# Kernel tuning notes

Hardware: AMD Instinct MI355X
Metric: run time of the kernel (lower is better)

## Reference

```python
import jax, jax.numpy as jnp
import numpy as np

N_NODES = 163842
N_EDGES = 983040
NUM_FEATURES = 22
LAYER_SIZES = [22, 32, 64, 64]
K = 3  # kernel_size
D = 2  # pseudo-coordinate dim
EPS = 1e-15


def _glorot(key, shape):
    fan = shape[0] + shape[-1]
    s = jnp.sqrt(6.0 / fan)
    return jax.random.uniform(key, shape, jnp.float32, -s, s)


def setup_inputs() -> dict:
    key = jax.random.key(0)
    ks = iter(jax.random.split(key, 64))
    inp = {
        'x': jax.random.normal(next(ks), (N_NODES, NUM_FEATURES), jnp.float32),
        'edge_index': jax.random.randint(next(ks), (2, N_EDGES), 0, N_NODES, jnp.int64),
        'edge_attr': jax.random.uniform(next(ks), (N_EDGES, D), jnp.float32),
    }
    for i, (cin, cout) in enumerate(zip(LAYER_SIZES[:-1], LAYER_SIZES[1:])):
        inp[f'g{i}'] = _glorot(next(ks), (cin, K * cout))
        inp[f'mu{i}'] = _glorot(next(ks), (K, D))
        inp[f'sigma{i}'] = jax.random.uniform(next(ks), (K, D), jnp.float32, 0.5, 1.5)
        inp[f'root{i}'] = _glorot(next(ks), (cin, cout))
        inp[f'b{i}'] = jnp.zeros((cout,), jnp.float32)
    inp['fc_w'] = _glorot(next(ks), (LAYER_SIZES[-1], 2))
    inp['fc_b'] = jnp.zeros((2,), jnp.float32)
    return inp


def gmm_conv(x, src, dst, pseudo, g, mu, sigma, root, bias):
    # PyG GMMConv, separate_gaussians=False, aggr='mean', root_weight=True
    n = x.shape[0]
    cout = root.shape[1]
    xw = (x @ g).reshape(n, K, cout)                       # [N, K, Cout]
    diff = pseudo[:, None, :] - mu[None, :, :]             # [E, K, D]
    gauss = jnp.exp(-0.5 * jnp.sum(diff * diff / (EPS + sigma[None] ** 2), axis=-1))  # [E, K]
    msg = jnp.einsum('ek,eko->eo', gauss, xw[src])         # [E, Cout]
    agg = jax.ops.segment_sum(msg, dst, num_segments=n)
    deg = jax.ops.segment_sum(jnp.ones((src.shape[0],), x.dtype), dst, num_segments=n)
    agg = agg / jnp.clip(deg, 1.0)[:, None]                # mean aggregation
    return agg + x @ root + bias


def reference(x, edge_index, edge_attr, g0, mu0, sigma0, root0, b0,
              g1, mu1, sigma1, root1, b1, g2, mu2, sigma2, root2, b2,
              fc_w, fc_b):
    src, dst = edge_index[0], edge_index[1]
    params = [(g0, mu0, sigma0, root0, b0),
              (g1, mu1, sigma1, root1, b1),
              (g2, mu2, sigma2, root2, b2)]
    h = x
    for (g, mu, sigma, root, b) in params:
        h = jax.nn.relu(gmm_conv(h, src, dst, edge_attr, g, mu, sigma, root, b))
    logits = h @ fc_w + fc_b                               # [N, 2]
    return jax.nn.log_softmax(logits, axis=1)
```

## Files before the change

### kernel.cpp

```cpp
#include <hip/hip_runtime.h>

#define NN 163842
#define NE 983040
#define NBIN 641
#define BINCAP 2048

using short8   = __attribute__((ext_vector_type(8))) short;
using ushort8v = __attribute__((ext_vector_type(8))) unsigned short;
using f32x4    = __attribute__((ext_vector_type(4))) float;
using v2f      = __attribute__((ext_vector_type(2))) float;

static __device__ __forceinline__ unsigned short bf16rne(float x) {
    unsigned u = __float_as_uint(x);
    u += 0x7FFFu + ((u >> 16) & 1u);
    return (unsigned short)(u >> 16);
}

static __device__ __forceinline__ v2f bfpair(unsigned u) {
    v2f r;
    r[0] = __uint_as_float(u << 16);
    r[1] = __uint_as_float(u & 0xffff0000u);
    return r;
}

__global__ __launch_bounds__(256) void bin_pass(const int* __restrict__ dst,
                                                const int* __restrict__ src,
                                                const float* __restrict__ ea,
                                                int* __restrict__ bincnt,
                                                int4* __restrict__ binbuf) {
    __shared__ int hist[NBIN], base[NBIN], pos[NBIN];
    const int t = threadIdx.x;
    for (int i = t; i < NBIN; i += 256) { hist[i] = 0; pos[i] = 0; }
    __syncthreads();
    const int e0 = blockIdx.x * 7680;
#pragma unroll 2
    for (int it = 0; it < 30; ++it) {
        int b = dst[e0 + it * 256 + t] >> 8;
        atomicAdd(&hist[b], 1);
    }
    __syncthreads();
    for (int i = t; i < NBIN; i += 256)
        if (hist[i] > 0) base[i] = atomicAdd(&bincnt[i], hist[i]);
    __syncthreads();
    for (int it = 0; it < 30; ++it) {
        int e = e0 + it * 256 + t;
        int d = dst[e];
        int b = d >> 8;
        int j = atomicAdd(&pos[b], 1);
        int slot = base[b] + j;
        float2 exy = *(const float2*)(ea + 2 * (size_t)e);
        int4 r;
        r.x = d; r.y = src[e];
        r.z = __float_as_int(exy.x); r.w = __float_as_int(exy.y);
        if (slot < BINCAP) binbuf[(size_t)b * BINCAP + slot] = r;
    }
}

__global__ void scan_bins(const int* __restrict__ bincnt, int* __restrict__ binoff) {
    __shared__ int tmp[1024];
    int t = threadIdx.x;
    int v = (t < NBIN) ? min(bincnt[t], BINCAP) : 0;
    tmp[t] = v;
    __syncthreads();
    for (int o = 1; o < 1024; o <<= 1) {
        int x = (t >= o) ? tmp[t - o] : 0;
        __syncthreads();
        tmp[t] += x;
        __syncthreads();
    }
    if (t < NBIN) binoff[t] = tmp[t] - v;
}

template <int CIN, int CINP, int COUTR>
static __device__ __forceinline__ void wcb_emit(int t, const float* __restrict__ g,
                                                const float* __restrict__ root,
                                                unsigned short* __restrict__ Wcb) {
    constexpr int KTl = 4 * CINP;
    int nIdx = t / KTl, k = t - nIdx * KTl;
    int seg = k / CINP, c = k - seg * CINP;
    float v = 0.0f;
    if (c < CIN)
        v = (seg < 3) ? g[c * (3 * COUTR) + seg * COUTR + nIdx] : root[c * COUTR + nIdx];
    Wcb[t] = bf16rne(v);
}

static __device__ __forceinline__ float3 gauss3c(float ex, float ey,
                                                 const float* muv, const float* ccv) {
    float3 r;
    float dx, dy;
    dx = ex - muv[0]; dy = ey - muv[1];
    r.x = __expf(fmaf(ccv[0] * dx, dx, ccv[1] * dy * dy));
    dx = ex - muv[2]; dy = ey - muv[3];
    r.y = __expf(fmaf(ccv[2] * dx, dx, ccv[3] * dy * dy));
    dx = ex - muv[4]; dy = ey - muv[5];
    r.z = __expf(fmaf(ccv[4] * dx, dx, ccv[5] * dy * dy));
    return r;
}

__global__ __launch_bounds__(256) void build_pass(const int4* __restrict__ binbuf,
                                                  const int* __restrict__ bincnt,
                                                  const int* __restrict__ binoff,
                                                  int* __restrict__ cnt,
                                                  int* __restrict__ cursor,
                                                  const float* __restrict__ mu0, const float* __restrict__ sg0,
                                                  const float* __restrict__ mu1, const float* __restrict__ sg1,
                                                  const float* __restrict__ mu2, const float* __restrict__ sg2,
                                                  float4* __restrict__ ged0,
                                                  float4* __restrict__ ged1,
                                                  float4* __restrict__ ged2,
                                                  const float* __restrict__ x,
                                                  unsigned short* __restrict__ xp,
                                                  const float* __restrict__ g0, const float* __restrict__ rt0,
                                                  const float* __restrict__ g1, const float* __restrict__ rt1,
                                                  const float* __restrict__ g2, const float* __restrict__ rt2,
                                                  unsigned short* __restrict__ W0,
                                                  unsigned short* __restrict__ W1,
                                                  unsigned short* __restrict__ W2,
                                                  int PBLK, int n) {
    __shared__ int h2[256], pre[256], pos2[256];
    const int t = threadIdx.x;
    int bid = blockIdx.x;
    if (bid < NBIN) {
        float muv0[6], ccv0[6], muv1[6], ccv1[6], muv2[6], ccv2[6];
#pragma unroll
        for (int j = 0; j < 6; ++j) {
            muv0[j] = mu0[j]; muv1[j] = mu1[j]; muv2[j] = mu2[j];
            float s0 = sg0[j], s1 = sg1[j], s2 = sg2[j];
            ccv0[j] = -0.5f / (1e-15f + s0 * s0);
            ccv1[j] = -0.5f / (1e-15f + s1 * s1);
            ccv2[j] = -0.5f / (1e-15f + s2 * s2);
        }
        const int total = min(bincnt[bid], BINCAP);
        const int boff  = binoff[bid];
        const int4* bb  = binbuf + (size_t)bid * BINCAP;
        h2[t] = 0; pos2[t] = 0;
        __syncthreads();
        for (int i = t; i < total; i += 256) atomicAdd(&h2[bb[i].x & 255], 1);
        __syncthreads();
        pre[t] = h2[t];
        __syncthreads();
        for (int o = 1; o < 256; o <<= 1) {
            int v = (t >= o) ? pre[t - o] : 0;
            __syncthreads();
            pre[t] += v;
            __syncthreads();
        }
        pre[t] -= h2[t];
        int node = (bid << 8) + t;
        if (node < n) { cnt[node] = h2[t]; cursor[node] = boff + pre[t]; }
        __syncthreads();
        for (int i = t; i < total; i += 256) {
            int4 r = bb[i];
            int l = r.x & 255;
            int j = atomicAdd(&pos2[l], 1);
            int p = boff + pre[l] + j;
            float exf = __int_as_float(r.z), eyf = __int_as_float(r.w);
            float sb  = __int_as_float(r.y);
            float3 G0 = gauss3c(exf, eyf, muv0, ccv0);
            float3 G1 = gauss3c(exf, eyf, muv1, ccv1);
            float3 G2 = gauss3c(exf, eyf, muv2, ccv2);
            ged0[p] = make_float4(sb, G0.x, G0.y, G0.z);
            ged1[p] = make_float4(sb, G1.x, G1.y, G1.z);
            ged2[p] = make_float4(sb, G2.x, G2.y, G2.z);
        }
        return;
    }
    bid -= NBIN;
    if (bid < PBLK) {
        int r = bid * 256 + threadIdx.x;
        if (r >= n) return;
        float v[22];
        const float2* x2 = (const float2*)(x + (size_t)r * 22);
#pragma unroll
        for (int j = 0; j < 11; ++j) *(float2*)(v + 2 * j) = x2[j];
        unsigned short* op = xp + (size_t)r * 32;
#pragma unroll
        for (int g8 = 0; g8 < 4; ++g8) {
            ushort8v o;
#pragma unroll
            for (int j = 0; j < 8; ++j) {
                int c = g8 * 8 + j;
                o[j] = (c < 22) ? bf16rne(v[c]) : (unsigned short)0;
            }
            *(ushort8v*)(op + g8 * 8) = o;
        }
        return;
    }
    bid -= PBLK;
    int tt = bid * 256 + threadIdx.x;
    constexpr int T0 = 32 * 128, T1 = 64 * 128, T2 = 64 * 256;
    if (tt < T0)                wcb_emit<22, 32, 32>(tt, g0, rt0, W0);
    else if (tt < T0 + T1)      wcb_emit<32, 32, 64>(tt - T0, g1, rt1, W1);
    else if (tt < T0 + T1 + T2) wcb_emit<64, 64, 64>(tt - T0 - T1, g2, rt2, W2);
}

template <int CINP, int COUTR, int NT, bool FC>
__global__ __launch_bounds__(NT) void fused_mfma(const unsigned short* __restrict__ h, int hs,
                                                 const float4* __restrict__ ged,
                                                 const int* __restrict__ cursor,
                                                 const int* __restrict__ degi,
                                                 const unsigned short* __restrict__ Wcb,
                                                 const float* __restrict__ bias,
                                                 unsigned short* __restrict__ out,
                                                 const float* __restrict__ fcw,
                                                 const float* __restrict__ fcb,
                                                 float* __restrict__ fout, int n) {
    constexpr int KT    = 4 * CINP;
    constexpr int ST4   = KT / 8 + 1;
    constexpr int ROWU  = ST4 * 8;
    constexpr int NSTEP = KT / 32;
    constexpr int NCT   = COUTR / 16;
    constexpr int LPN   = CINP / 8;
    constexpr int NPP   = NT / LPN;
    static_assert(NPP == 64, "single pass over the 64-node tile");
    __shared__ float4 sa[64 * ST4];
    unsigned short* st = (unsigned short*)sa;
    const int row0 = blockIdx.x * 64;

    {
        const int sub = threadIdx.x / LPN;
        const int li  = threadIdx.x % LPN;
        int node = row0 + sub; if (node > n - 1) node = n - 1;
        int p   = cursor[node];
        int dg  = degi[node];
        int end = p + dg;
        v2f a[3][4];
#pragma unroll
        for (int k = 0; k < 3; ++k)
#pragma unroll
            for (int q = 0; q < 4; ++q) a[k][q] = (v2f){0.0f, 0.0f};
        for (; p < end; p += 4) {
            float4 ed[4];
            uint4  hu[4];
#pragma unroll
            for (int u = 0; u < 4; ++u) {
                int q = p + u;
                ed[u] = ged[(q < end) ? q : (end - 1)];
            }
#pragma unroll
            for (int u = 0; u < 4; ++u)
                hu[u] = *(const uint4*)(h + (long)__float_as_int(ed[u].x) * hs + li * 8);
#pragma unroll
            for (int u = 0; u < 4; ++u)
                if (p + u >= end) { ed[u].y = 0.0f; ed[u].z = 0.0f; ed[u].w = 0.0f; }
#pragma unroll
            for (int u = 0; u < 4; ++u) {
                v2f hv[4] = {bfpair(hu[u].x), bfpair(hu[u].y), bfpair(hu[u].z), bfpair(hu[u].w)};
#pragma unroll
                for (int q = 0; q < 4; ++q) {
                    a[0][q] += hv[q] * ed[u].y;
                    a[1][q] += hv[q] * ed[u].z;
                    a[2][q] += hv[q] * ed[u].w;
                }
            }
        }
        float inv = 1.0f / (float)max(dg, 1);
#pragma unroll
        for (int k = 0; k < 3; ++k)
#pragma unroll
            for (int q = 0; q < 4; ++q) a[k][q] *= inv;
        uint4 hv4 = *(const uint4*)(h + (long)node * hs + li * 8);
        int base = sub * ROWU;
        int c8b  = li * 8;
#pragma unroll
        for (int k = 0; k < 3; ++k) {
            ushort8v v;
#pragma unroll
            for (int q = 0; q < 4; ++q) {
                v[2 * q]     = bf16rne(a[k][q][0]);
                v[2 * q + 1] = bf16rne(a[k][q][1]);
            }
            *(ushort8v*)(st + base + k * CINP + c8b) = v;
        }
        *(uint4*)(st + base + 3 * CINP + c8b) = hv4;
    }
    __syncthreads();

    constexpr int NW    = NT / 64;
    constexpr int TILES = 4 * NCT;
    constexpr int TPW   = TILES / NW;
    constexpr int RST   = NW / NCT;
    static_assert(NW % NCT == 0 && TILES % NW == 0, "tile remap");
    const int lane = threadIdx.x & 63;
    const int wv   = threadIdx.x >> 6;
    const int quad = lane >> 4;
    const int c16  = lane & 15;
    const int ct   = wv % NCT;
    const int rg0  = wv / NCT;
    f32x4 acc[TPW];
#pragma unroll
    for (int i = 0; i < TPW; ++i) acc[i] = (f32x4){0.0f, 0.0f, 0.0f, 0.0f};
    const unsigned short* bcol = Wcb + (ct * 16 + c16) * KT;
#pragma unroll
    for (int s = 0; s < NSTEP; ++s) {
        short8 bf = *(const short8*)(bcol + s * 32 + quad * 8);
#pragma unroll
        for (int i = 0; i < TPW; ++i) {
            const unsigned short* arow = st + (16 * (rg0 + i * RST) + c16) * ROWU;
            short8 af = *(const short8*)(arow + s * 32 + quad * 8);
            acc[i] = __builtin_amdgcn_mfma_f32_16x16x32_bf16(af, bf, acc[i], 0, 0, 0);
        }
    }
    if constexpr (!FC) {
#pragma unroll
        for (int i = 0; i < TPW; ++i) {
            int rg  = rg0 + i * RST;
            int col = ct * 16 + c16;
            float b = bias[col];
#pragma unroll
            for (int r = 0; r < 4; ++r) {
                int grow = row0 + rg * 16 + quad * 4 + r;
                if (grow < n)
                    out[(long)grow * COUTR + col] = bf16rne(fmaxf(acc[i][r] + b, 0.0f));
            }
        }
    } else {
        static_assert(COUTR == 64, "FC fusion assumes 64-wide rows");
        constexpr int FS = 72;
        __syncthreads();
        {
            int col = ct * 16 + c16;
            float b = bias[col];
#pragma unroll
            for (int i = 0; i < TPW; ++i) {
                int rg = rg0 + i * RST;
#pragma unroll
                for (int r = 0; r < 4; ++r) {
                    int lr2 = rg * 16 + quad * 4 + r;
                    st[lr2 * FS + col] = bf16rne(fmaxf(acc[i][r] + b, 0.0f));
                }
            }
        }
        __syncthreads();
        int t = threadIdx.x;
        if (t < 64) {
            int node = row0 + t;
            if (node < n) {
                const ushort8v* hr = (const ushort8v*)(st + t * FS);
                float l0 = fcb[0];
                float l1 = fcb[1];
#pragma unroll
                for (int j8 = 0; j8 < 8; ++j8) {
                    ushort8v hv = hr[j8];
#pragma unroll
                    for (int j = 0; j < 8; ++j) {
                        float hvf = __uint_as_float(((unsigned)hv[j]) << 16);
                        l0 = fmaf(hvf, fcw[2 * (8 * j8 + j)], l0);
                        l1 = fmaf(hvf, fcw[2 * (8 * j8 + j) + 1], l1);
                    }
                }
                float mx  = fmaxf(l0, l1);
                float lse = mx + logf(__expf(l0 - mx) + __expf(l1 - mx));
                fout[2 * (long)node]     = l0 - lse;
                fout[2 * (long)node + 1] = l1 - lse;
            }
        }
    }
}

extern "C" void kernel_launch(void* const* d_in, const int* in_sizes, int n_in,
                              void* d_out, int out_size, void* d_ws, size_t ws_size,
                              hipStream_t stream) {
    const float* x   = (const float*)d_in[0];
    const int*   ei  = (const int*)d_in[1];
    const float* ea  = (const float*)d_in[2];
    const float* g_[3]  = {(const float*)d_in[3],  (const float*)d_in[8],  (const float*)d_in[13]};
    const float* mu_[3] = {(const float*)d_in[4],  (const float*)d_in[9],  (const float*)d_in[14]};
    const float* sg_[3] = {(const float*)d_in[5],  (const float*)d_in[10], (const float*)d_in[15]};
    const float* rt_[3] = {(const float*)d_in[6],  (const float*)d_in[11], (const float*)d_in[16]};
    const float* bs_[3] = {(const float*)d_in[7],  (const float*)d_in[12], (const float*)d_in[17]};
    const float* fcw = (const float*)d_in[18];
    const float* fcb = (const float*)d_in[19];
    float* out = (float*)d_out;
    (void)in_sizes; (void)n_in; (void)out_size; (void)ws_size;

    char* w = (char*)d_ws;
    size_t off = 0;
    auto carve = [&](size_t bytes) -> void* {
        void* p = (void*)(w + off);
        off += (bytes + 255) & ~(size_t)255;
        return p;
    };
    int*    cnt    = (int*)carve((size_t)NN * 4);
    int*    cursor = (int*)carve((size_t)NN * 4);
    int*    bincnt = (int*)carve((size_t)NBIN * 4);
    int*    binoff = (int*)carve((size_t)NBIN * 4);
    float4* ged0   = (float4*)carve((size_t)NE * 16);
    float4* ged1   = (float4*)carve((size_t)NE * 16);
    float4* ged2   = (float4*)carve((size_t)NE * 16);
    unsigned short* W0 = (unsigned short*)carve((size_t)32 * 128 * 2);
    unsigned short* W1 = (unsigned short*)carve((size_t)64 * 128 * 2);
    unsigned short* W2 = (unsigned short*)carve((size_t)64 * 256 * 2);
    unsigned short* xp = (unsigned short*)carve((size_t)NN * 32 * 2);
    char* uni = (char*)carve((size_t)NN * 64 * 2 + (size_t)NN * 32 * 2);
    int4*           binbuf = (int4*)uni;
    unsigned short* hA     = (unsigned short*)uni;
    unsigned short* hB     = (unsigned short*)(uni + (size_t)NN * 32 * 2);

    const int* src = ei;
    const int* dst = ei + NE;
    const int PB = (NN + 255) / 256;
    const int WB = 112;
    const int GB = (NN + 63) / 64;

    hipMemsetAsync(bincnt, 0, (size_t)NBIN * 4, stream);
    bin_pass<<<128, 256, 0, stream>>>(dst, src, ea, bincnt, binbuf);
    scan_bins<<<1, 1024, 0, stream>>>(bincnt, binoff);
    build_pass<<<NBIN + PB + WB, 256, 0, stream>>>(binbuf, bincnt, binoff, cnt, cursor,
                                                   mu_[0], sg_[0], mu_[1], sg_[1], mu_[2], sg_[2],
                                                   ged0, ged1, ged2, x, xp,
                                                   g_[0], rt_[0], g_[1], rt_[1], g_[2], rt_[2],
                                                   W0, W1, W2, PB, NN);

    fused_mfma<32, 32, 256, false><<<GB, 256, 0, stream>>>(xp, 32, ged0, cursor, cnt,
                                                           W0, bs_[0], hA, nullptr, nullptr,
                                                           nullptr, NN);
    fused_mfma<32, 64, 256, false><<<GB, 256, 0, stream>>>(hA, 32, ged1, cursor, cnt,
                                                           W1, bs_[1], hB, nullptr, nullptr,
                                                           nullptr, NN);
    fused_mfma<64, 64, 512, true><<<GB, 512, 0, stream>>>(hB, 64, ged2, cursor, cnt,
                                                          W2, bs_[2], nullptr, fcw, fcb,
                                                          out, NN);
}
```

Measured before the change: 283.0 us.

## Fold bin offset scan into build pass and double bin_pass grid

Removes the separate single-block scan_bins launch. Each build_pass bin block now computes its own offset by reducing the preceding bin counts in shared memory. bin_pass launches twice as many blocks with half the edges each, and the gather loop predicates out-of-range edge and feature loads instead of clamping. This saves one launch and serialization point, at the cost of redundant prefix reads in every bin block.

```diff
diff --git a/kernel.cpp b/kernel.cpp
--- a/kernel.cpp
+++ b/kernel.cpp
@@ -32,9 +32,9 @@
     const int t = threadIdx.x;
     for (int i = t; i < NBIN; i += 256) { hist[i] = 0; pos[i] = 0; }
     __syncthreads();
-    const int e0 = blockIdx.x * 7680;
-#pragma unroll 2
-    for (int it = 0; it < 30; ++it) {
+    const int e0 = blockIdx.x * 3840;
+#pragma unroll 3
+    for (int it = 0; it < 15; ++it) {
         int b = dst[e0 + it * 256 + t] >> 8;
         atomicAdd(&hist[b], 1);
     }
@@ -42,7 +42,7 @@
     for (int i = t; i < NBIN; i += 256)
         if (hist[i] > 0) base[i] = atomicAdd(&bincnt[i], hist[i]);
     __syncthreads();
-    for (int it = 0; it < 30; ++it) {
+    for (int it = 0; it < 15; ++it) {
         int e = e0 + it * 256 + t;
         int d = dst[e];
         int b = d >> 8;
@@ -54,21 +54,6 @@
         r.z = __float_as_int(exy.x); r.w = __float_as_int(exy.y);
         if (slot < BINCAP) binbuf[(size_t)b * BINCAP + slot] = r;
     }
-}
-
-__global__ void scan_bins(const int* __restrict__ bincnt, int* __restrict__ binoff) {
-    __shared__ int tmp[1024];
-    int t = threadIdx.x;
-    int v = (t < NBIN) ? min(bincnt[t], BINCAP) : 0;
-    tmp[t] = v;
-    __syncthreads();
-    for (int o = 1; o < 1024; o <<= 1) {
-        int x = (t >= o) ? tmp[t - o] : 0;
-        __syncthreads();
-        tmp[t] += x;
-        __syncthreads();
-    }
-    if (t < NBIN) binoff[t] = tmp[t] - v;
 }
 
 template <int CIN, int CINP, int COUTR>
@@ -99,7 +84,6 @@
 
 __global__ __launch_bounds__(256) void build_pass(const int4* __restrict__ binbuf,
                                                   const int* __restrict__ bincnt,
-                                                  const int* __restrict__ binoff,
                                                   int* __restrict__ cnt,
                                                   int* __restrict__ cursor,
                                                   const float* __restrict__ mu0, const float* __restrict__ sg0,
@@ -121,6 +105,16 @@
     const int t = threadIdx.x;
     int bid = blockIdx.x;
     if (bid < NBIN) {
+        int partial = 0;
+        for (int i = t; i < bid; i += 256) partial += min(bincnt[i], BINCAP);
+        pre[t] = partial;
+        __syncthreads();
+        for (int o = 128; o > 0; o >>= 1) {
+            if (t < o) pre[t] += pre[t + o];
+            __syncthreads();
+        }
+        const int boff = pre[0];
+
         float muv0[6], ccv0[6], muv1[6], ccv1[6], muv2[6], ccv2[6];
 #pragma unroll
         for (int j = 0; j < 6; ++j) {
@@ -131,7 +125,6 @@
             ccv2[j] = -0.5f / (1e-15f + s2 * s2);
         }
         const int total = min(bincnt[bid], BINCAP);
-        const int boff  = binoff[bid];
         const int4* bb  = binbuf + (size_t)bid * BINCAP;
         h2[t] = 0; pos2[t] = 0;
         __syncthreads();
@@ -234,15 +227,16 @@
             uint4  hu[4];
 #pragma unroll
             for (int u = 0; u < 4; ++u) {
-                int q = p + u;
-                ed[u] = ged[(q < end) ? q : (end - 1)];
-            }
-#pragma unroll
-            for (int u = 0; u < 4; ++u)
-                hu[u] = *(const uint4*)(h + (long)__float_as_int(ed[u].x) * hs + li * 8);
-#pragma unroll
-            for (int u = 0; u < 4; ++u)
-                if (p + u >= end) { ed[u].y = 0.0f; ed[u].z = 0.0f; ed[u].w = 0.0f; }
+                if (p + u < end) ed[u] = ged[p + u];
+                else             ed[u] = make_float4(0.0f, 0.0f, 0.0f, 0.0f);
+            }
+#pragma unroll
+            for (int u = 0; u < 4; ++u) {
+                if (p + u < end)
+                    hu[u] = *(const uint4*)(h + (long)__float_as_int(ed[u].x) * hs + li * 8);
+                else
+                    hu[u] = (uint4){0u, 0u, 0u, 0u};
+            }
 #pragma unroll
             for (int u = 0; u < 4; ++u) {
                 v2f hv[4] = {bfpair(hu[u].x), bfpair(hu[u].y), bfpair(hu[u].z), bfpair(hu[u].w)};
@@ -384,7 +378,6 @@
     int*    cnt    = (int*)carve((size_t)NN * 4);
     int*    cursor = (int*)carve((size_t)NN * 4);
     int*    bincnt = (int*)carve((size_t)NBIN * 4);
-    int*    binoff = (int*)carve((size_t)NBIN * 4);
     float4* ged0   = (float4*)carve((size_t)NE * 16);
     float4* ged1   = (float4*)carve((size_t)NE * 16);
     float4* ged2   = (float4*)carve((size_t)NE * 16);
@@ -404,9 +397,8 @@
     const int GB = (NN + 63) / 64;
 
     hipMemsetAsync(bincnt, 0, (size_t)NBIN * 4, stream);
-    bin_pass<<<128, 256, 0, stream>>>(dst, src, ea, bincnt, binbuf);
-    scan_bins<<<1, 1024, 0, stream>>>(bincnt, binoff);
-    build_pass<<<NBIN + PB + WB, 256, 0, stream>>>(binbuf, bincnt, binoff, cnt, cursor,
+    bin_pass<<<256, 256, 0, stream>>>(dst, src, ea, bincnt, binbuf);
+    build_pass<<<NBIN + PB + WB, 256, 0, stream>>>(binbuf, bincnt, cnt, cursor,
                                                    mu_[0], sg_[0], mu_[1], sg_[1], mu_[2], sg_[2],
                                                    ged0, ged1, ged2, x, xp,
                                                    g_[0], rt_[0], g_[1], rt_[1], g_[2], rt_[2],
```

Result: slower. 293.4 us (+3.7%).
